# Kernel optimization log

Hardware: AMD Instinct MI355X
Metric: run time of the kernel (lower is better)

## Reference

```python
import jax, jax.numpy as jnp
import numpy as np

B, C, A, H, W = 8, 64, 32, 64, 64  # batch, input_nf, atten_nf, height, width

def setup_inputs() -> dict:
    key = jax.random.key(0)
    k = jax.random.split(key, 5)
    scale = 1.0 / np.sqrt(C)
    return {
        "x":  jax.random.normal(k[0], (B, C, H, W), dtype=jnp.float32),
        "Wg": jax.random.uniform(k[1], (A, C), jnp.float32, -scale, scale),  # 1x1 conv kernel
        "bg": jax.random.uniform(k[2], (A,),   jnp.float32, -scale, scale),
        "Wh": jax.random.uniform(k[3], (A, C), jnp.float32, -scale, scale),
        "bh": jax.random.uniform(k[4], (A,),   jnp.float32, -scale, scale),
    }

def reference(x, Wg, bg, Wh, bh):
    b, c, h, w = x.shape
    n = h * w
    xf = x.reshape(b, c, n)                               # [B, C, N]
    g = jnp.einsum('ac,bcn->ban', Wg, xf) + bg[None, :, None]  # 1x1 conv == GEMM
    hq = jnp.einsum('ac,bcn->ban', Wh, xf) + bh[None, :, None]
    scores = jnp.einsum('ban,bam->bnm', g, hq)            # [B, N, N]
    alpha = jax.nn.softmax(scores, axis=2)
    r = jnp.einsum('bnm,bcm->bcn', alpha, xf)             # alpha @ x^T, back to [B,C,N]
    r = r.reshape(b, c, h, w)
    r = r + x  # is_residual=True
    return (jax.nn.relu(r), alpha)
```

## Files before the change

kernel.cpp:

```cpp
#include <hip/hip_runtime.h>
#include <hip/hip_bf16.h>
#include <math.h>

#define NB 8
#define NC 64
#define NA 32
#define NN 4096
#define NWAVE 8

typedef __attribute__((ext_vector_type(8))) short bf16x8;
typedef __attribute__((ext_vector_type(4))) float f32x4;

__device__ inline ushort f2bf(float f) {
  union { float f; unsigned u; } v; v.f = f;
  unsigned r = v.u + 0x7fffu + ((v.u >> 16) & 1u);
  return (ushort)(r >> 16);
}

__device__ inline uint2 packbf(const f32x4 p) {
  uint2 q;
  q.x = (uint)f2bf(p[0]) | ((uint)f2bf(p[1]) << 16);
  q.y = (uint)f2bf(p[2]) | ((uint)f2bf(p[3]) << 16);
  return q;
}

__global__ __launch_bounds__(256) void prep_kernel(
    const float* __restrict__ x, const float* __restrict__ Wg, const float* __restrict__ bg,
    const float* __restrict__ Wh, const float* __restrict__ bh,
    ushort* __restrict__ gT, ushort* __restrict__ hqT, ushort* __restrict__ xfb)
{
  __shared__ float wg_s[NA * NC];
  __shared__ float wh_s[NA * NC];
  const int t = threadIdx.x;
  for (int i = t; i < NA * NC; i += 256) { wg_s[i] = Wg[i]; wh_s[i] = Wh[i]; }
  __syncthreads();

  const int gid = blockIdx.x * 256 + t;
  const int b = gid >> 12;
  const int n = gid & (NN - 1);
  const float* xb = x + (size_t)b * NC * NN + n;

  float accg[NA], acch[NA];
#pragma unroll
  for (int a = 0; a < NA; ++a) { accg[a] = 0.f; acch[a] = 0.f; }

  for (int c4 = 0; c4 < NC / 4; ++c4) {
    const float xv0 = xb[(size_t)(c4 * 4 + 0) * NN];
    const float xv1 = xb[(size_t)(c4 * 4 + 1) * NN];
    const float xv2 = xb[(size_t)(c4 * 4 + 2) * NN];
    const float xv3 = xb[(size_t)(c4 * 4 + 3) * NN];
    const size_t xo = ((size_t)b * NC + c4 * 4) * NN + n;
    xfb[xo]          = f2bf(xv0);
    xfb[xo + NN]     = f2bf(xv1);
    xfb[xo + 2 * NN] = f2bf(xv2);
    xfb[xo + 3 * NN] = f2bf(xv3);
#pragma unroll
    for (int a = 0; a < NA; ++a) {
      const float4 wg4 = *(const float4*)&wg_s[a * NC + c4 * 4];
      const float4 wh4 = *(const float4*)&wh_s[a * NC + c4 * 4];
      accg[a] += wg4.x * xv0 + wg4.y * xv1 + wg4.z * xv2 + wg4.w * xv3;
      acch[a] += wh4.x * xv0 + wh4.y * xv1 + wh4.z * xv2 + wh4.w * xv3;
    }
  }

  const float LOG2E = 1.44269504088896340736f;
  ushort og[NA], oh[NA];
#pragma unroll
  for (int a = 0; a < NA; ++a) {
    og[a] = f2bf((accg[a] + bg[a]) * LOG2E);
    oh[a] = f2bf(acch[a] + bh[a]);
  }
  const size_t o = ((size_t)b * NN + n) * NA;
#pragma unroll
  for (int k = 0; k < 4; ++k) {
    uint4 vg, vh;
    vg.x = (uint)og[k*8+0] | ((uint)og[k*8+1] << 16);
    vg.y = (uint)og[k*8+2] | ((uint)og[k*8+3] << 16);
    vg.z = (uint)og[k*8+4] | ((uint)og[k*8+5] << 16);
    vg.w = (uint)og[k*8+6] | ((uint)og[k*8+7] << 16);
    vh.x = (uint)oh[k*8+0] | ((uint)oh[k*8+1] << 16);
    vh.y = (uint)oh[k*8+2] | ((uint)oh[k*8+3] << 16);
    vh.z = (uint)oh[k*8+4] | ((uint)oh[k*8+5] << 16);
    vh.w = (uint)oh[k*8+6] | ((uint)oh[k*8+7] << 16);
    *(uint4*)(gT  + o + k * 8) = vg;
    *(uint4*)(hqT + o + k * 8) = vh;
  }
}

__global__ __launch_bounds__(512, 4) void attn_kernel(
    const ushort* __restrict__ gT, const ushort* __restrict__ hqT,
    const ushort* __restrict__ xfb, const float* __restrict__ x,
    float* __restrict__ outp, float* __restrict__ alpha)
{
  __shared__ ushort pbuf[NWAVE][32][36];
  __shared__ float rtile[32][65];
  __shared__ float Lp[NWAVE][32];

  const int tid = threadIdx.x;
  const int l  = tid & 63;
  const int w  = tid >> 6;
  const int lm = l & 15;
  const int lh = l >> 4;
  const int b  = blockIdx.x >> 7;
  const int n0 = (blockIdx.x & 127) << 5;
  const int mbase = w << 9;

  const ushort* gB = gT  + (size_t)b * NN * NA;
  const ushort* hB = hqT + (size_t)b * NN * NA;
  const ushort* xB = xfb + (size_t)b * NC * NN;

  bf16x8 gb0 = *(const bf16x8*)(gB + (size_t)(n0 + lm) * NA + lh * 8);
  bf16x8 gb1 = *(const bf16x8*)(gB + (size_t)(n0 + 16 + lm) * NA + lh * 8);
  bf16x8 ha0 = *(const bf16x8*)(hB + (size_t)(mbase + lm) * NA + lh * 8);
  bf16x8 ha1 = *(const bf16x8*)(hB + (size_t)(mbase + 16 + lm) * NA + lh * 8);

  float* rflat = &rtile[0][0];
  for (int i = tid; i < 32 * 65; i += 512) rflat[i] = 0.f;

  const f32x4 zz = {0.f, 0.f, 0.f, 0.f};

  float sume0 = 0.f, sume1 = 0.f;
  for (int mc = 0; mc < 16; ++mc) {
    const int m1 = mbase + (((mc + 1) & 15) << 5);
    const bf16x8 na0 = *(const bf16x8*)(hB + (size_t)(m1 + lm) * NA + lh * 8);
    const bf16x8 na1 = *(const bf16x8*)(hB + (size_t)(m1 + 16 + lm) * NA + lh * 8);

    const f32x4 s00 = __builtin_amdgcn_mfma_f32_16x16x32_bf16(ha0, gb0, zz, 0, 0, 0);
    const f32x4 s10 = __builtin_amdgcn_mfma_f32_16x16x32_bf16(ha1, gb0, zz, 0, 0, 0);
    const f32x4 s01 = __builtin_amdgcn_mfma_f32_16x16x32_bf16(ha0, gb1, zz, 0, 0, 0);
    const f32x4 s11 = __builtin_amdgcn_mfma_f32_16x16x32_bf16(ha1, gb1, zz, 0, 0, 0);
#pragma unroll
    for (int r = 0; r < 4; ++r) {
      sume0 += exp2f(s00[r]) + exp2f(s10[r]);
      sume1 += exp2f(s01[r]) + exp2f(s11[r]);
    }
    ha0 = na0; ha1 = na1;
  }
  sume0 += __shfl_xor(sume0, 16); sume0 += __shfl_xor(sume0, 32);
  sume1 += __shfl_xor(sume1, 16); sume1 += __shfl_xor(sume1, 32);
  if (l < 16) { Lp[w][l] = sume0; Lp[w][16 + l] = sume1; }
  __syncthreads();

  float Ls0 = 0.f, Ls1 = 0.f;
#pragma unroll
  for (int ww = 0; ww < NWAVE; ++ww) { Ls0 += Lp[ww][lm]; Ls1 += Lp[ww][16 + lm]; }
  const float Linv0 = 1.0f / Ls0;
  const float Linv1 = 1.0f / Ls1;

  f32x4 racc[2][4];
#pragma unroll
  for (int gi = 0; gi < 2; ++gi)
#pragma unroll
    for (int ci = 0; ci < 4; ++ci) racc[gi][ci] = zz;

  float* aB = alpha + ((size_t)b * NN + n0) * NN;

  for (int mc = 0; mc < 16; ++mc) {
    const int m0 = mbase + (mc << 5);
    const int m1 = mbase + (((mc + 1) & 15) << 5);
    const bf16x8 na0 = *(const bf16x8*)(hB + (size_t)(m1 + lm) * NA + lh * 8);
    const bf16x8 na1 = *(const bf16x8*)(hB + (size_t)(m1 + 16 + lm) * NA + lh * 8);

    const f32x4 s00 = __builtin_amdgcn_mfma_f32_16x16x32_bf16(ha0, gb0, zz, 0, 0, 0);
    const f32x4 s10 = __builtin_amdgcn_mfma_f32_16x16x32_bf16(ha1, gb0, zz, 0, 0, 0);
    const f32x4 s01 = __builtin_amdgcn_mfma_f32_16x16x32_bf16(ha0, gb1, zz, 0, 0, 0);
    const f32x4 s11 = __builtin_amdgcn_mfma_f32_16x16x32_bf16(ha1, gb1, zz, 0, 0, 0);

    f32x4 p00, p10, p01, p11;
#pragma unroll
    for (int r = 0; r < 4; ++r) {
      p00[r] = exp2f(s00[r]) * Linv0;
      p10[r] = exp2f(s10[r]) * Linv0;
      p01[r] = exp2f(s01[r]) * Linv1;
      p11[r] = exp2f(s11[r]) * Linv1;
    }

    __builtin_nontemporal_store(p00, (f32x4*)(aB + (size_t)lm * NN        + m0 + lh * 4));
    __builtin_nontemporal_store(p10, (f32x4*)(aB + (size_t)lm * NN        + m0 + 16 + lh * 4));
    __builtin_nontemporal_store(p01, (f32x4*)(aB + (size_t)(16 + lm) * NN + m0 + lh * 4));
    __builtin_nontemporal_store(p11, (f32x4*)(aB + (size_t)(16 + lm) * NN + m0 + 16 + lh * 4));

    *(uint2*)&pbuf[w][lm][lh * 4]           = packbf(p00);
    *(uint2*)&pbuf[w][lm][16 + lh * 4]      = packbf(p10);
    *(uint2*)&pbuf[w][16 + lm][lh * 4]      = packbf(p01);
    *(uint2*)&pbuf[w][16 + lm][16 + lh * 4] = packbf(p11);

    union UB { uint4 u; bf16x8 v; } ua, ub;
    {
      const uint2 a0 = *(const uint2*)&pbuf[w][lm][lh * 8];
      const uint2 a1 = *(const uint2*)&pbuf[w][lm][lh * 8 + 4];
      ua.u = make_uint4(a0.x, a0.y, a1.x, a1.y);
      const uint2 b0 = *(const uint2*)&pbuf[w][16 + lm][lh * 8];
      const uint2 b1 = *(const uint2*)&pbuf[w][16 + lm][lh * 8 + 4];
      ub.u = make_uint4(b0.x, b0.y, b1.x, b1.y);
    }
    const bf16x8 pa0 = ua.v;
    const bf16x8 pa1 = ub.v;

#pragma unroll
    for (int ci = 0; ci < 4; ++ci) {
      const bf16x8 xv = *(const bf16x8*)(xB + (size_t)(ci * 16 + lm) * NN + m0 + lh * 8);
      racc[0][ci] = __builtin_amdgcn_mfma_f32_16x16x32_bf16(pa0, xv, racc[0][ci], 0, 0, 0);
      racc[1][ci] = __builtin_amdgcn_mfma_f32_16x16x32_bf16(pa1, xv, racc[1][ci], 0, 0, 0);
    }
    ha0 = na0; ha1 = na1;
  }

#pragma unroll
  for (int gi = 0; gi < 2; ++gi)
#pragma unroll
    for (int ci = 0; ci < 4; ++ci)
#pragma unroll
      for (int r = 0; r < 4; ++r)
        atomicAdd(&rtile[gi * 16 + lh * 4 + r][ci * 16 + lm], racc[gi][ci][r]);
  __syncthreads();

  const int c  = tid >> 3;
  const int j4 = (tid & 7) << 2;
  f32x4 v;
#pragma unroll
  for (int k = 0; k < 4; ++k) v[k] = rtile[j4 + k][c];
  const size_t oo = ((size_t)b * NC + c) * NN + n0 + j4;
  const f32x4 xr = *(const f32x4*)(x + oo);
#pragma unroll
  for (int k = 0; k < 4; ++k) {
    const float t = v[k] + xr[k];
    v[k] = t > 0.f ? t : 0.f;
  }
  __builtin_nontemporal_store(v, (f32x4*)(outp + oo));
}

extern "C" void kernel_launch(void* const* d_in, const int* in_sizes, int n_in,
                              void* d_out, int out_size, void* d_ws, size_t ws_size,
                              hipStream_t stream) {
  const float* x  = (const float*)d_in[0];
  const float* Wg = (const float*)d_in[1];
  const float* bg = (const float*)d_in[2];
  const float* Wh = (const float*)d_in[3];
  const float* bh = (const float*)d_in[4];

  float* outp  = (float*)d_out;
  float* alpha = outp + (size_t)NB * NC * NN;

  ushort* gT  = (ushort*)d_ws;
  ushort* hqT = gT + (size_t)NB * NN * NA;
  ushort* xfb = hqT + (size_t)NB * NN * NA;

  prep_kernel<<<NB * NN / 256, 256, 0, stream>>>(x, Wg, bg, Wh, bh, gT, hqT, xfb);
  attn_kernel<<<NB * (NN / 32), 512, 0, stream>>>(gT, hqT, xfb, x, outp, alpha);
}
```

Before: 235.3 us.

## Split attention into unnormalized rsum kernel and separate alpha-write kernel

```diff
diff --git a/kernel.cpp b/kernel.cpp
--- a/kernel.cpp
+++ b/kernel.cpp
@@ -87,7 +87,7 @@
   }
 }
 
-__global__ __launch_bounds__(512, 4) void attn_kernel(
+__global__ __launch_bounds__(512, 4) void rsum_kernel(
     const ushort* __restrict__ gT, const ushort* __restrict__ hqT,
     const ushort* __restrict__ xfb, const float* __restrict__ x,
     float* __restrict__ outp, float* __restrict__ alpha)
@@ -95,15 +95,17 @@
   __shared__ ushort pbuf[NWAVE][32][36];
   __shared__ float rtile[32][65];
   __shared__ float Lp[NWAVE][32];
+  __shared__ float LinvS[32];
 
   const int tid = threadIdx.x;
   const int l  = tid & 63;
   const int w  = tid >> 6;
   const int lm = l & 15;
   const int lh = l >> 4;
-  const int b  = blockIdx.x >> 7;
-  const int n0 = (blockIdx.x & 127) << 5;
-  const int mbase = w << 9;
+
+  const int wgid = (blockIdx.x & 7) * 128 + (blockIdx.x >> 3);
+  const int b  = wgid >> 7;
+  const int n0 = (wgid & 127) << 5;
 
   const ushort* gB = gT  + (size_t)b * NN * NA;
   const ushort* hB = hqT + (size_t)b * NN * NA;
@@ -111,79 +113,52 @@
 
   bf16x8 gb0 = *(const bf16x8*)(gB + (size_t)(n0 + lm) * NA + lh * 8);
   bf16x8 gb1 = *(const bf16x8*)(gB + (size_t)(n0 + 16 + lm) * NA + lh * 8);
-  bf16x8 ha0 = *(const bf16x8*)(hB + (size_t)(mbase + lm) * NA + lh * 8);
-  bf16x8 ha1 = *(const bf16x8*)(hB + (size_t)(mbase + 16 + lm) * NA + lh * 8);
+  const int mfirst = w << 9;
+  bf16x8 ha0 = *(const bf16x8*)(hB + (size_t)(mfirst + lm) * NA + lh * 8);
+  bf16x8 ha1 = *(const bf16x8*)(hB + (size_t)(mfirst + 16 + lm) * NA + lh * 8);
 
   float* rflat = &rtile[0][0];
   for (int i = tid; i < 32 * 65; i += 512) rflat[i] = 0.f;
 
   const f32x4 zz = {0.f, 0.f, 0.f, 0.f};
+  f32x4 racc[2][4];
+#pragma unroll
+  for (int gi = 0; gi < 2; ++gi)
+#pragma unroll
+    for (int ci = 0; ci < 4; ++ci) racc[gi][ci] = zz;
 
   float sume0 = 0.f, sume1 = 0.f;
+
   for (int mc = 0; mc < 16; ++mc) {
-    const int m1 = mbase + (((mc + 1) & 15) << 5);
+    const int m0 = (w << 9) + (mc << 5);
+    const int m1 = (w << 9) + (((mc + 1) & 15) << 5);
     const bf16x8 na0 = *(const bf16x8*)(hB + (size_t)(m1 + lm) * NA + lh * 8);
     const bf16x8 na1 = *(const bf16x8*)(hB + (size_t)(m1 + 16 + lm) * NA + lh * 8);
+    bf16x8 xv[4];
+#pragma unroll
+    for (int ci = 0; ci < 4; ++ci)
+      xv[ci] = *(const bf16x8*)(xB + (size_t)(ci * 16 + lm) * NN + m0 + lh * 8);
 
     const f32x4 s00 = __builtin_amdgcn_mfma_f32_16x16x32_bf16(ha0, gb0, zz, 0, 0, 0);
     const f32x4 s10 = __builtin_amdgcn_mfma_f32_16x16x32_bf16(ha1, gb0, zz, 0, 0, 0);
     const f32x4 s01 = __builtin_amdgcn_mfma_f32_16x16x32_bf16(ha0, gb1, zz, 0, 0, 0);
     const f32x4 s11 = __builtin_amdgcn_mfma_f32_16x16x32_bf16(ha1, gb1, zz, 0, 0, 0);
+
+    f32x4 e00, e10, e01, e11;
 #pragma unroll
     for (int r = 0; r < 4; ++r) {
-      sume0 += exp2f(s00[r]) + exp2f(s10[r]);
-      sume1 += exp2f(s01[r]) + exp2f(s11[r]);
-    }
-    ha0 = na0; ha1 = na1;
-  }
-  sume0 += __shfl_xor(sume0, 16); sume0 += __shfl_xor(sume0, 32);
-  sume1 += __shfl_xor(sume1, 16); sume1 += __shfl_xor(sume1, 32);
-  if (l < 16) { Lp[w][l] = sume0; Lp[w][16 + l] = sume1; }
-  __syncthreads();
-
-  float Ls0 = 0.f, Ls1 = 0.f;
-#pragma unroll
-  for (int ww = 0; ww < NWAVE; ++ww) { Ls0 += Lp[ww][lm]; Ls1 += Lp[ww][16 + lm]; }
-  const float Linv0 = 1.0f / Ls0;
-  const float Linv1 = 1.0f / Ls1;
-
-  f32x4 racc[2][4];
-#pragma unroll
-  for (int gi = 0; gi < 2; ++gi)
-#pragma unroll
-    for (int ci = 0; ci < 4; ++ci) racc[gi][ci] = zz;
-
-  float* aB = alpha + ((size_t)b * NN + n0) * NN;
-
-  for (int mc = 0; mc < 16; ++mc) {
-    const int m0 = mbase + (mc << 5);
-    const int m1 = mbase + (((mc + 1) & 15) << 5);
-    const bf16x8 na0 = *(const bf16x8*)(hB + (size_t)(m1 + lm) * NA + lh * 8);
-    const bf16x8 na1 = *(const bf16x8*)(hB + (size_t)(m1 + 16 + lm) * NA + lh * 8);
-
-    const f32x4 s00 = __builtin_amdgcn_mfma_f32_16x16x32_bf16(ha0, gb0, zz, 0, 0, 0);
-    const f32x4 s10 = __builtin_amdgcn_mfma_f32_16x16x32_bf16(ha1, gb0, zz, 0, 0, 0);
-    const f32x4 s01 = __builtin_amdgcn_mfma_f32_16x16x32_bf16(ha0, gb1, zz, 0, 0, 0);
-    const f32x4 s11 = __builtin_amdgcn_mfma_f32_16x16x32_bf16(ha1, gb1, zz, 0, 0, 0);
-
-    f32x4 p00, p10, p01, p11;
-#pragma unroll
-    for (int r = 0; r < 4; ++r) {
-      p00[r] = exp2f(s00[r]) * Linv0;
-      p10[r] = exp2f(s10[r]) * Linv0;
-      p01[r] = exp2f(s01[r]) * Linv1;
-      p11[r] = exp2f(s11[r]) * Linv1;
-    }
-
-    __builtin_nontemporal_store(p00, (f32x4*)(aB + (size_t)lm * NN        + m0 + lh * 4));
-    __builtin_nontemporal_store(p10, (f32x4*)(aB + (size_t)lm * NN        + m0 + 16 + lh * 4));
-    __builtin_nontemporal_store(p01, (f32x4*)(aB + (size_t)(16 + lm) * NN + m0 + lh * 4));
-    __builtin_nontemporal_store(p11, (f32x4*)(aB + (size_t)(16 + lm) * NN + m0 + 16 + lh * 4));
-
-    *(uint2*)&pbuf[w][lm][lh * 4]           = packbf(p00);
-    *(uint2*)&pbuf[w][lm][16 + lh * 4]      = packbf(p10);
-    *(uint2*)&pbuf[w][16 + lm][lh * 4]      = packbf(p01);
-    *(uint2*)&pbuf[w][16 + lm][16 + lh * 4] = packbf(p11);
+      e00[r] = exp2f(s00[r]);
+      e10[r] = exp2f(s10[r]);
+      e01[r] = exp2f(s01[r]);
+      e11[r] = exp2f(s11[r]);
+      sume0 += e00[r] + e10[r];
+      sume1 += e01[r] + e11[r];
+    }
+
+    *(uint2*)&pbuf[w][lm][lh * 4]           = packbf(e00);
+    *(uint2*)&pbuf[w][lm][16 + lh * 4]      = packbf(e10);
+    *(uint2*)&pbuf[w][16 + lm][lh * 4]      = packbf(e01);
+    *(uint2*)&pbuf[w][16 + lm][16 + lh * 4] = packbf(e11);
 
     union UB { uint4 u; bf16x8 v; } ua, ub;
     {
@@ -194,16 +169,27 @@
       const uint2 b1 = *(const uint2*)&pbuf[w][16 + lm][lh * 8 + 4];
       ub.u = make_uint4(b0.x, b0.y, b1.x, b1.y);
     }
-    const bf16x8 pa0 = ua.v;
-    const bf16x8 pa1 = ub.v;
 
 #pragma unroll
     for (int ci = 0; ci < 4; ++ci) {
-      const bf16x8 xv = *(const bf16x8*)(xB + (size_t)(ci * 16 + lm) * NN + m0 + lh * 8);
-      racc[0][ci] = __builtin_amdgcn_mfma_f32_16x16x32_bf16(pa0, xv, racc[0][ci], 0, 0, 0);
-      racc[1][ci] = __builtin_amdgcn_mfma_f32_16x16x32_bf16(pa1, xv, racc[1][ci], 0, 0, 0);
+      racc[0][ci] = __builtin_amdgcn_mfma_f32_16x16x32_bf16(ua.v, xv[ci], racc[0][ci], 0, 0, 0);
+      racc[1][ci] = __builtin_amdgcn_mfma_f32_16x16x32_bf16(ub.v, xv[ci], racc[1][ci], 0, 0, 0);
     }
     ha0 = na0; ha1 = na1;
+  }
+
+  sume0 += __shfl_xor(sume0, 16); sume0 += __shfl_xor(sume0, 32);
+  sume1 += __shfl_xor(sume1, 16); sume1 += __shfl_xor(sume1, 32);
+  if (l < 16) { Lp[w][l] = sume0; Lp[w][16 + l] = sume1; }
+  __syncthreads();
+
+  if (tid < 32) {
+    float s = 0.f;
+#pragma unroll
+    for (int ww = 0; ww < NWAVE; ++ww) s += Lp[ww][tid];
+    const float li = 1.0f / s;
+    LinvS[tid] = li;
+    alpha[((size_t)b * NN + n0 + tid) * NN] = li;
   }
 
 #pragma unroll
@@ -219,7 +205,7 @@
   const int j4 = (tid & 7) << 2;
   f32x4 v;
 #pragma unroll
-  for (int k = 0; k < 4; ++k) v[k] = rtile[j4 + k][c];
+  for (int k = 0; k < 4; ++k) v[k] = rtile[j4 + k][c] * LinvS[j4 + k];
   const size_t oo = ((size_t)b * NC + c) * NN + n0 + j4;
   const f32x4 xr = *(const f32x4*)(x + oo);
 #pragma unroll
@@ -228,6 +214,66 @@
     v[k] = t > 0.f ? t : 0.f;
   }
   __builtin_nontemporal_store(v, (f32x4*)(outp + oo));
+}
+
+__global__ __launch_bounds__(512, 4) void alpha_kernel(
+    const ushort* __restrict__ gT, const ushort* __restrict__ hqT,
+    float* __restrict__ alpha)
+{
+  const int tid = threadIdx.x;
+  const int l  = tid & 63;
+  const int w  = tid >> 6;
+  const int lm = l & 15;
+  const int lh = l >> 4;
+
+  const int wgid = (blockIdx.x & 7) * 128 + (blockIdx.x >> 3);
+  const int b  = wgid >> 7;
+  const int n0 = (wgid & 127) << 5;
+
+  const ushort* gB = gT  + (size_t)b * NN * NA;
+  const ushort* hB = hqT + (size_t)b * NN * NA;
+  float* aB = alpha + ((size_t)b * NN + n0) * NN;
+
+  const float Linv0 = aB[(size_t)lm * NN];
+  const float Linv1 = aB[(size_t)(16 + lm) * NN];
+
+  bf16x8 gb0 = *(const bf16x8*)(gB + (size_t)(n0 + lm) * NA + lh * 8);
+  bf16x8 gb1 = *(const bf16x8*)(gB + (size_t)(n0 + 16 + lm) * NA + lh * 8);
+  const int mfirst = w << 9;
+  bf16x8 ha0 = *(const bf16x8*)(hB + (size_t)(mfirst + lm) * NA + lh * 8);
+  bf16x8 ha1 = *(const bf16x8*)(hB + (size_t)(mfirst + 16 + lm) * NA + lh * 8);
+
+  __syncthreads();
+
+  const f32x4 zz = {0.f, 0.f, 0.f, 0.f};
+
+  for (int mc = 0; mc < 16; ++mc) {
+    const int m0 = (w << 9) + (mc << 5);
+    const int m1 = (w << 9) + (((mc + 1) & 15) << 5);
+    const bf16x8 na0 = *(const bf16x8*)(hB + (size_t)(m1 + lm) * NA + lh * 8);
+    const bf16x8 na1 = *(const bf16x8*)(hB + (size_t)(m1 + 16 + lm) * NA + lh * 8);
+
+    const f32x4 s00 = __builtin_amdgcn_mfma_f32_16x16x32_bf16(ha0, gb0, zz, 0, 0, 0);
+    const f32x4 s10 = __builtin_amdgcn_mfma_f32_16x16x32_bf16(ha1, gb0, zz, 0, 0, 0);
+    const f32x4 s01 = __builtin_amdgcn_mfma_f32_16x16x32_bf16(ha0, gb1, zz, 0, 0, 0);
+    const f32x4 s11 = __builtin_amdgcn_mfma_f32_16x16x32_bf16(ha1, gb1, zz, 0, 0, 0);
+
+    f32x4 p00, p10, p01, p11;
+#pragma unroll
+    for (int r = 0; r < 4; ++r) {
+      p00[r] = exp2f(s00[r]) * Linv0;
+      p10[r] = exp2f(s10[r]) * Linv0;
+      p01[r] = exp2f(s01[r]) * Linv1;
+      p11[r] = exp2f(s11[r]) * Linv1;
+    }
+
+    *(f32x4*)(aB + (size_t)lm * NN        + m0 + lh * 4)      = p00;
+    *(f32x4*)(aB + (size_t)lm * NN        + m0 + 16 + lh * 4) = p10;
+    *(f32x4*)(aB + (size_t)(16 + lm) * NN + m0 + lh * 4)      = p01;
+    *(f32x4*)(aB + (size_t)(16 + lm) * NN + m0 + 16 + lh * 4) = p11;
+
+    ha0 = na0; ha1 = na1;
+  }
 }
 
 extern "C" void kernel_launch(void* const* d_in, const int* in_sizes, int n_in,
@@ -247,5 +293,6 @@
   ushort* xfb = hqT + (size_t)NB * NN * NA;
 
   prep_kernel<<<NB * NN / 256, 256, 0, stream>>>(x, Wg, bg, Wh, bh, gT, hqT, xfb);
-  attn_kernel<<<NB * (NN / 32), 512, 0, stream>>>(gT, hqT, xfb, x, outp, alpha);
-}
+  rsum_kernel<<<NB * (NN / 32), 512, 0, stream>>>(gT, hqT, xfb, x, outp, alpha);
+  alpha_kernel<<<NB * (NN / 32), 512, 0, stream>>>(gT, hqT, alpha);
+}
```

Result: slower. 332.8 us (+41.5%).
